# Kernel tuning notes

Measured on AMD Instinct MI355X. Metric: run time of the kernel, lower is better.

## Reference

```python
import jax, jax.numpy as jnp
import numpy as np

N = 50000      # nodes
E = 1600000    # edges (avg degree 32)
F_IN = 128
F_OUT = 64
ALPHA = 0.2    # LeakyReLU negative slope


def setup_inputs() -> dict:
    key = jax.random.key(0)
    ks = jax.random.split(key, 11)
    xav = 1.414 * (2.0 / (F_IN + F_OUT)) ** 0.5  # xavier_normal gain=1.414
    xav_a = 1.414 * (2.0 / (1 + 2 * F_OUT)) ** 0.5
    return {
        "input": jax.random.normal(ks[0], (N, F_IN), jnp.float32),
        "p_h": jax.random.normal(ks[1], (N, F_IN), jnp.float32),
        "new_h": jax.random.normal(ks[2], (N, F_IN), jnp.float32),
        "edge": jax.random.randint(ks[3], (2, E), 0, N),
        "edge_col": jax.random.randint(ks[4], (2, N), 0, N),
        "row_i": jax.random.randint(ks[5], (N,), 0, N),
        "row_resort": jax.random.randint(ks[6], (E,), 0, N),
        "adj": jnp.zeros((1,), jnp.float32),  # unused by forward (kept for signature parity)
        "W": jax.random.normal(ks[7], (F_IN, F_OUT), jnp.float32) * xav,
        "a1": jax.random.normal(ks[8], (1, 2 * F_OUT), jnp.float32) * xav_a,
        "a2": jax.random.normal(ks[9], (1, 2 * F_OUT), jnp.float32) * xav_a,
    }


def segment_softmax(src, index, num_segments):
    # torch_geometric.utils.softmax: numerically-stable softmax grouped by index
    m = jax.ops.segment_max(src, index, num_segments=num_segments)
    m = jnp.where(jnp.isfinite(m), m, 0.0)  # empty segments -> 0
    ex = jnp.exp(src - m[index])
    s = jax.ops.segment_sum(ex, index, num_segments=num_segments)
    return ex / (s[index] + 1e-16)


def reference(input, p_h, new_h, edge, edge_col, row_i, row_resort, adj, W, a1, a2):
    n = input.shape[0]
    fo = W.shape[1]
    h = input @ W            # [N, Fo]
    ph = p_h @ W             # [N, Fo]
    nh = new_h @ W           # [N, Fo]

    # a1 @ cat(h_src, p_h).T  ==  h_src @ a1_left + p_h @ a1_right  (avoids [E,2Fo] concat)
    a1l, a1r = a1[0, :fo], a1[0, fo:]
    col_score = h[edge_col[0]] @ a1l + ph @ a1r                 # [N]
    edge_col_e = jnp.exp(-jax.nn.leaky_relu(col_score, ALPHA))
    edge_col_e = segment_softmax(edge_col_e, row_i, n)

    a2l, a2r = a2[0, :fo], a2[0, fo:]
    row_score = nh[row_resort] @ a2l + h[edge[1]] @ a2r          # [E]
    edge_row_e = jnp.exp(-jax.nn.leaky_relu(row_score, ALPHA))

    edge_e = edge_row_e * edge_col_e[row_resort]                 # [E]

    # special_spmm(edge, edge_e, [N,N], ones) == segment row-sum
    e_rowsum = jax.ops.segment_sum(edge_e, edge[0], num_segments=n)[:, None]  # [N,1]
    e_rowsum = e_rowsum + jnp.where(e_rowsum == 0, 1.0, 0.0)

    attention_e = edge_e[:, None] / e_rowsum[edge[0]]            # [E,1]

    # dropout p=0.0 (eval): identity
    # special_spmm(edge, edge_e, [N,N], h) == segment-weighted aggregate
    h_prime = jax.ops.segment_sum(edge_e[:, None] * h[edge[1]], edge[0], num_segments=n)
    h_prime = h_prime / e_rowsum

    return jax.nn.elu(h_prime), edge, attention_e
```

## Files before the change

kernel.cpp:

```cpp
#include <hip/hip_runtime.h>

#define NN 50000
#define NE 1600000
#define FIN 128
#define FOUT 64
#define ALPHA 0.2f

#define RANGE 256
#define NB 196
#define EPB 2048
#define NBLK 782

__global__ void k_sniff(const int* __restrict__ edge32, int* __restrict__ iflag) {
    __shared__ int zodd;
    if (threadIdx.x == 0) zodd = 0;
    __syncthreads();
    int z = 0;
    for (int i = threadIdx.x; i < 2048; i += 256)
        if (edge32[2 * i + 1] == 0) z++;
    atomicAdd(&zodd, z);
    __syncthreads();
    if (threadIdx.x == 0) *iflag = (zodd > 2000) ? 1 : 0;
}

__device__ inline int ldi(const void* p, size_t i, int isi64) {
    int v = isi64 ? (int)((const long long*)p)[i] : ((const int*)p)[i];
    return v < 0 ? 0 : (v >= NN ? NN - 1 : v);
}

__device__ inline unsigned short f2bf(float x) {
    unsigned u = __float_as_uint(x);
    return (unsigned short)((u + 0x7FFFu + ((u >> 16) & 1u)) >> 16);
}

__global__ void k_u(const float* __restrict__ W, const float* __restrict__ a1,
                    const float* __restrict__ a2, float* __restrict__ u) {
    int k = threadIdx.x;
    float u1 = 0.f, u2 = 0.f, u3 = 0.f, u4 = 0.f;
    for (int j = 0; j < FOUT; j++) {
        float w = W[k * FOUT + j];
        u1 += w * a1[j];
        u2 += w * a1[FOUT + j];
        u3 += w * a2[j];
        u4 += w * a2[FOUT + j];
    }
    u[k] = u1; u[128 + k] = u2; u[256 + k] = u3; u[384 + k] = u4;
}

__global__ __launch_bounds__(256) void k_gemm(const float* __restrict__ X,
                                              const float* __restrict__ W,
                                              unsigned short* __restrict__ h) {
    __shared__ float wlds[FIN * FOUT];
    __shared__ float xlds[4][4][FIN];
    int tid = threadIdx.x;
    for (int i = tid; i < FIN * FOUT; i += 256) wlds[i] = W[i];
    int wave = tid >> 6, lane = tid & 63;
    int base = blockIdx.x * 16 + wave * 4;
    for (int n0 = 0; n0 < 4; n0++) {
        float2 b = ((const float2*)(X + (size_t)(base + n0) * FIN))[lane];
        xlds[wave][n0][2 * lane] = b.x;
        xlds[wave][n0][2 * lane + 1] = b.y;
    }
    __syncthreads();
    float a0 = 0.f, a1v = 0.f, a2v = 0.f, a3 = 0.f;
    for (int k = 0; k < FIN; k++) {
        float w = wlds[k * FOUT + lane];
        a0  += xlds[wave][0][k] * w;
        a1v += xlds[wave][1][k] * w;
        a2v += xlds[wave][2][k] * w;
        a3  += xlds[wave][3][k] * w;
    }
    h[(size_t)(base + 0) * FOUT + lane] = f2bf(a0);
    h[(size_t)(base + 1) * FOUT + lane] = f2bf(a1v);
    h[(size_t)(base + 2) * FOUT + lane] = f2bf(a2v);
    h[(size_t)(base + 3) * FOUT + lane] = f2bf(a3);
}

__global__ __launch_bounds__(256) void k_svec(const float* __restrict__ input,
                                              const float* __restrict__ p_h,
                                              const float* __restrict__ new_h,
                                              const float* __restrict__ u,
                                              float* __restrict__ s1, float* __restrict__ s2,
                                              float* __restrict__ sc ,
                                              float* __restrict__ s4) {
    int lane = threadIdx.x & 63;
    int v = blockIdx.x * 4 + (threadIdx.x >> 6);
    size_t row = (size_t)v * FIN;
    float2 bi = ((const float2*)(input + row))[lane];
    float2 bp = ((const float2*)(p_h   + row))[lane];
    float2 bn = ((const float2*)(new_h + row))[lane];
    float p1 = bi.x * u[2 * lane]       + bi.y * u[2 * lane + 1];
    float p2 = bp.x * u[128 + 2 * lane] + bp.y * u[128 + 2 * lane + 1];
    float p3 = bn.x * u[256 + 2 * lane] + bn.y * u[256 + 2 * lane + 1];
    float p4 = bi.x * u[384 + 2 * lane] + bi.y * u[384 + 2 * lane + 1];
#pragma unroll
    for (int off = 32; off > 0; off >>= 1) {
        p1 += __shfl_down(p1, off, 64);
        p2 += __shfl_down(p2, off, 64);
        p3 += __shfl_down(p3, off, 64);
        p4 += __shfl_down(p4, off, 64);
    }
    if (lane == 0) { s1[v] = p1; s2[v] = p2; sc[2 * v] = p3; s4[v] = p4; }
}

__global__ void k_colscore(const float* __restrict__ s1, const float* __restrict__ s2,
                           const void* __restrict__ edge_col, const void* __restrict__ row_i,
                           const int* __restrict__ iflag,
                           float* __restrict__ ec, unsigned int* __restrict__ m) {
    int i = blockIdx.x * 256 + threadIdx.x;
    if (i >= NN) return;
    int i64 = *iflag;
    float cs = s1[ldi(edge_col, i, i64)] + s2[i];
    float l = cs > 0.f ? cs : ALPHA * cs;
    float e = expf(-l);
    ec[i] = e;
    atomicMax(&m[ldi(row_i, i, i64)], __float_as_uint(e));
}

__global__ void k_expsum(float* __restrict__ ec, const unsigned int* __restrict__ m,
                         const void* __restrict__ row_i, const int* __restrict__ iflag,
                         float* __restrict__ ssum) {
    int i = blockIdx.x * 256 + threadIdx.x;
    if (i >= NN) return;
    int r = ldi(row_i, i, *iflag);
    float e = expf(ec[i] - __uint_as_float(m[r]));
    ec[i] = e;
    atomicAdd(&ssum[r], e);
}

__global__ void k_norm(const float* __restrict__ ex, const float* __restrict__ ssum,
                       const void* __restrict__ row_i, const int* __restrict__ iflag,
                       float* __restrict__ sc ) {
    int i = blockIdx.x * 256 + threadIdx.x;
    if (i >= NN) return;
    sc[2 * i + 1] = ex[i] / (ssum[ldi(row_i, i, *iflag)] + 1e-16f);
}

__global__ __launch_bounds__(512) void k_cnt(const void* __restrict__ edge,
                                             const int* __restrict__ iflag,
                                             int* __restrict__ cntm) {
    __shared__ int hist[NB];
    int tid = threadIdx.x;
    for (int t = tid; t < NB; t += 512) hist[t] = 0;
    __syncthreads();
    int i64 = *iflag;
    int base = blockIdx.x * EPB;
#pragma unroll
    for (int k = 0; k < 4; k++) {
        int e = base + k * 512 + tid;
        if (e < NE) atomicAdd(&hist[ldi(edge, e, i64) >> 8], 1);
    }
    __syncthreads();
    for (int t = tid; t < NB; t += 512)
        cntm[blockIdx.x * NB + t] = hist[t];
}

__global__ __launch_bounds__(1024) void k_colscan(const int* __restrict__ cntm,
                                                  int* __restrict__ colpre,
                                                  int* __restrict__ bcnt) {
    __shared__ int s[1024];
    int b = blockIdx.x, tid = threadIdx.x;
    int x = (tid < NBLK) ? cntm[(size_t)tid * NB + b] : 0;
    s[tid] = x;
    __syncthreads();
    for (int off = 1; off < 1024; off <<= 1) {
        int t = (tid >= off) ? s[tid - off] : 0;
        __syncthreads();
        s[tid] += t;
        __syncthreads();
    }
    if (tid < NBLK) colpre[(size_t)tid * NB + b] = s[tid] - x;
    if (tid == 1023) bcnt[b] = s[1023];
}

__global__ __launch_bounds__(256) void k_bscan(const int* __restrict__ bcnt,
                                               int* __restrict__ bstart,
                                               int* __restrict__ start) {
    __shared__ int s[256];
    int tid = threadIdx.x;
    int x = (tid < NB) ? bcnt[tid] : 0;
    s[tid] = x;
    __syncthreads();
    for (int off = 1; off < 256; off <<= 1) {
        int t = (tid >= off) ? s[tid - off] : 0;
        __syncthreads();
        s[tid] += t;
        __syncthreads();
    }
    if (tid < NB) bstart[tid] = s[tid] - x;
    if (tid == 0) { bstart[NB] = NE; start[NN] = NE; }
}

__global__ __launch_bounds__(512) void k_edgeA(const float2* __restrict__ sc, const float* __restrict__ s4,
                                               const void* __restrict__ edge, const void* __restrict__ row_resort,
                                               const int* __restrict__ iflag,
                                               const int* __restrict__ bstart, const int* __restrict__ colpre,
                                               uint2* __restrict__ tmp,
                                               float* __restrict__ edge_e ) {
    __shared__ int hist[NB];
    __shared__ int bbase[NB];
    int tid = threadIdx.x;
    for (int t = tid; t < NB; t += 512) hist[t] = 0;
    __syncthreads();
    int i64 = *iflag;
    int base = blockIdx.x * EPB;
    unsigned int key[4]; float val[4]; int rk[4], bk[4];
#pragma unroll
    for (int k = 0; k < 4; k++) {
        int e = base + k * 512 + tid;
        bk[k] = -1;
        if (e < NE) {
            int e0 = ldi(edge, e, i64);
            int e1 = ldi(edge, (size_t)NE + e, i64);
            int rr = ldi(row_resort, e, i64);
            float2 c = sc[rr];
            float rs = c.x + s4[e1];
            float l = rs > 0.f ? rs : ALPHA * rs;
            float ee = expf(-l) * c.y;
            edge_e[e] = ee;
            key[k] = (unsigned int)e0 | ((unsigned int)e1 << 16);
            val[k] = ee;
            bk[k] = e0 >> 8;
            rk[k] = atomicAdd(&hist[bk[k]], 1);
        }
    }
    __syncthreads();
    for (int t = tid; t < NB; t += 512)
        bbase[t] = bstart[t] + colpre[(size_t)blockIdx.x * NB + t];
    __syncthreads();
#pragma unroll
    for (int k = 0; k < 4; k++)
        if (bk[k] >= 0)
            tmp[bbase[bk[k]] + rk[k]] = make_uint2(key[k], __float_as_uint(val[k]));
}

__global__ __launch_bounds__(512) void k_edgeB(const uint2* __restrict__ tmp,
                                               const int* __restrict__ bstart,
                                               int* __restrict__ start,
                                               float2* __restrict__ pairs) {
    __shared__ int cnt[RANGE];
    __shared__ int s[RANGE];
    __shared__ int cur[RANGE];
    int b = blockIdx.x;
    int tid = threadIdx.x;
    int v0 = b * RANGE;
    if (tid < RANGE) cnt[tid] = 0;
    __syncthreads();
    int lo = bstart[b], hi = bstart[b + 1];
    for (int i = lo + tid; i < hi; i += 512)
        atomicAdd(&cnt[tmp[i].x & 0xFFu], 1);
    __syncthreads();
    if (tid < RANGE) s[tid] = cnt[tid];
    __syncthreads();
    for (int off = 1; off < RANGE; off <<= 1) {
        int t = 0;
        if (tid < RANGE && tid >= off) t = s[tid - off];
        __syncthreads();
        if (tid < RANGE) s[tid] += t;
        __syncthreads();
    }
    if (tid < RANGE) {
        int g = lo + s[tid] - cnt[tid];
        cur[tid] = g;
        int v = v0 + tid;
        if (v < NN) start[v] = g;
    }
    __syncthreads();
    for (int i = lo + tid; i < hi; i += 512) {
        uint2 r = tmp[i];
        int pos = atomicAdd(&cur[r.x & 0xFFu], 1);
        pairs[pos] = make_float2(__int_as_float((int)(r.x >> 16)), __uint_as_float(r.y));
    }
}

__global__ __launch_bounds__(512) void k_agg(const unsigned short* __restrict__ h,
                                             const float2* __restrict__ pairs,
                                             const int* __restrict__ start,
                                             float* __restrict__ ersum,
                                             float* __restrict__ out0) {
    int lane = threadIdx.x & 63;
    int q  = lane >> 4;
    int fq = lane & 15;
    int v = blockIdx.x * 8 + (threadIdx.x >> 6);
    int a = start[v], b = start[v + 1];
    float acc0 = 0.f, acc1 = 0.f, acc2 = 0.f, acc3 = 0.f, rs = 0.f;
    for (int j = a; j < b; j += 8) {
        int eA = j + q, eB = j + 4 + q;
        float2 pA = (eA < b) ? pairs[eA] : make_float2(__int_as_float(0), 0.f);
        float2 pB = (eB < b) ? pairs[eB] : make_float2(__int_as_float(0), 0.f);
        uint2 hA = *(const uint2*)(h + (((size_t)__float_as_int(pA.x)) << 6) + 4 * fq);
        uint2 hB = *(const uint2*)(h + (((size_t)__float_as_int(pB.x)) << 6) + 4 * fq);
        acc0 += pA.y * __uint_as_float(hA.x << 16);
        acc1 += pA.y * __uint_as_float(hA.x & 0xFFFF0000u);
        acc2 += pA.y * __uint_as_float(hA.y << 16);
        acc3 += pA.y * __uint_as_float(hA.y & 0xFFFF0000u);
        acc0 += pB.y * __uint_as_float(hB.x << 16);
        acc1 += pB.y * __uint_as_float(hB.x & 0xFFFF0000u);
        acc2 += pB.y * __uint_as_float(hB.y << 16);
        acc3 += pB.y * __uint_as_float(hB.y & 0xFFFF0000u);
        rs += pA.y + pB.y;
    }
#pragma unroll
    for (int off = 16; off <= 32; off <<= 1) {
        acc0 += __shfl_xor(acc0, off, 64);
        acc1 += __shfl_xor(acc1, off, 64);
        acc2 += __shfl_xor(acc2, off, 64);
        acc3 += __shfl_xor(acc3, off, 64);
        rs   += __shfl_xor(rs, off, 64);
    }
    if (q == 0) {
        rs += (rs == 0.f) ? 1.f : 0.f;
        float4 o;
        o.x = acc0 / rs; o.y = acc1 / rs; o.z = acc2 / rs; o.w = acc3 / rs;
        o.x = o.x > 0.f ? o.x : expm1f(o.x);
        o.y = o.y > 0.f ? o.y : expm1f(o.y);
        o.z = o.z > 0.f ? o.z : expm1f(o.z);
        o.w = o.w > 0.f ? o.w : expm1f(o.w);
        ((float4*)(out0 + (size_t)v * FOUT))[fq] = o;
        if (fq == 0) ersum[v] = rs;
    }
}

__global__ __launch_bounds__(256) void k_final(const void* __restrict__ edge, const int* __restrict__ iflag,
                                               const float* __restrict__ ersum,
                                               float* __restrict__ out2, float* __restrict__ out1) {
    int i = blockIdx.x * 256 + threadIdx.x;
    int i64 = *iflag;
    int v = i64 ? (int)((const long long*)edge)[i] : ((const int*)edge)[i];
    out1[i] = (float)v;
    if (i < NE) {
        int e0 = v < 0 ? 0 : (v >= NN ? NN - 1 : v);
        out2[i] = out2[i] / ersum[e0];
    }
}

extern "C" void kernel_launch(void* const* d_in, const int* in_sizes, int n_in,
                              void* d_out, int out_size, void* d_ws, size_t ws_size,
                              hipStream_t stream) {
    int ix[3] = {0, 1, 2}; int nx = 0;
    int iE = 3, iCol = 4, iRowI = 5, iRes = 6, iW = 8, iA1 = 9, iA2 = 10;
    bool a1seen = false;
    for (int i = 0; i < n_in; i++) {
        int s = in_sizes[i];
        if (s == NN * FIN) { if (nx < 3) ix[nx++] = i; }
        else if (s == 2 * NE) iE = i;
        else if (s == 2 * NN) iCol = i;
        else if (s == NN) iRowI = i;
        else if (s == NE) iRes = i;
        else if (s == FIN * FOUT) iW = i;
        else if (s == 2 * FOUT) { if (!a1seen) { iA1 = i; a1seen = true; } else iA2 = i; }
    }
    const float* input = (const float*)d_in[ix[0]];
    const float* p_h   = (const float*)d_in[ix[1]];
    const float* new_h = (const float*)d_in[ix[2]];
    const void* edge       = d_in[iE];
    const void* edge_col   = d_in[iCol];
    const void* row_i      = d_in[iRowI];
    const void* row_resort = d_in[iRes];
    const float* W  = (const float*)d_in[iW];
    const float* a1 = (const float*)d_in[iA1];
    const float* a2 = (const float*)d_in[iA2];

    float* out0 = (float*)d_out;
    float* out1 = out0 + (size_t)NN * FOUT;
    float* out2 = out1 + (size_t)2 * NE;

    uint2* tmp = (uint2*)out1;

    unsigned short* h = (unsigned short*)d_ws;
    float2* pairs  = (float2*)((float*)d_ws + (size_t)NN * FOUT);
    float*  s1     = (float*)(pairs + NE);
    float*  s2     = s1 + NN;
    float*  s4     = s2 + NN;
    float*  ec     = s4 + NN;
    float*  scf    = ec + NN;
    float*  mseg   = scf + 2 * (size_t)NN;
    float*  ssum   = mseg + NN;
    int*    bcnt   = (int*)(ssum + NN);
    int*    start  = bcnt + NB;
    int*    bstart = start + NN + 1;
    int*    cntm   = bstart + NB + 1;
    int*    colpre = cntm + (size_t)NBLK * NB;
    float*  ersum  = (float*)(colpre + (size_t)NBLK * NB);
    float*  u      = ersum + NN;
    int*    iflag  = (int*)(u + 512);

    hipMemsetAsync(mseg, 0, (size_t)2 * NN * sizeof(float), stream);

    k_sniff<<<1, 256, 0, stream>>>((const int*)edge, iflag);
    k_u<<<1, 128, 0, stream>>>(W, a1, a2, u);
    k_gemm<<<NN / 16, 256, 0, stream>>>(input, W, h);
    k_svec<<<NN / 4, 256, 0, stream>>>(input, p_h, new_h, u, s1, s2, scf, s4);
    k_colscore<<<(NN + 255) / 256, 256, 0, stream>>>(s1, s2, edge_col, row_i, iflag, ec, (unsigned int*)mseg);
    k_expsum<<<(NN + 255) / 256, 256, 0, stream>>>(ec, (const unsigned int*)mseg, row_i, iflag, ssum);
    k_norm<<<(NN + 255) / 256, 256, 0, stream>>>(ec, ssum, row_i, iflag, scf);
    k_cnt<<<NBLK, 512, 0, stream>>>(edge, iflag, cntm);
    k_colscan<<<NB, 1024, 0, stream>>>(cntm, colpre, bcnt);
    k_bscan<<<1, 256, 0, stream>>>(bcnt, bstart, start);
    k_edgeA<<<NBLK, 512, 0, stream>>>((const float2*)scf, s4, edge, row_resort, iflag, bstart, colpre, tmp, out2);
    k_edgeB<<<NB, 512, 0, stream>>>(tmp, bstart, start, pairs);
    k_agg<<<NN / 8, 512, 0, stream>>>(h, pairs, start, ersum, out0);
    k_final<<<2 * NE / 256, 256, 0, stream>>>(edge, iflag, ersum, out2, out1);
}
```

Before: 310.7 us.

## Merge small setup kernels, fuse edge histogram into svec, widen agg gathers

```diff
diff --git a/kernel.cpp b/kernel.cpp
--- a/kernel.cpp
+++ b/kernel.cpp
@@ -11,18 +11,6 @@
 #define EPB 2048
 #define NBLK 782
 
-__global__ void k_sniff(const int* __restrict__ edge32, int* __restrict__ iflag) {
-    __shared__ int zodd;
-    if (threadIdx.x == 0) zodd = 0;
-    __syncthreads();
-    int z = 0;
-    for (int i = threadIdx.x; i < 2048; i += 256)
-        if (edge32[2 * i + 1] == 0) z++;
-    atomicAdd(&zodd, z);
-    __syncthreads();
-    if (threadIdx.x == 0) *iflag = (zodd > 2000) ? 1 : 0;
-}
-
 __device__ inline int ldi(const void* p, size_t i, int isi64) {
     int v = isi64 ? (int)((const long long*)p)[i] : ((const int*)p)[i];
     return v < 0 ? 0 : (v >= NN ? NN - 1 : v);
@@ -33,18 +21,33 @@
     return (unsigned short)((u + 0x7FFFu + ((u >> 16) & 1u)) >> 16);
 }
 
-__global__ void k_u(const float* __restrict__ W, const float* __restrict__ a1,
-                    const float* __restrict__ a2, float* __restrict__ u) {
-    int k = threadIdx.x;
-    float u1 = 0.f, u2 = 0.f, u3 = 0.f, u4 = 0.f;
-    for (int j = 0; j < FOUT; j++) {
-        float w = W[k * FOUT + j];
-        u1 += w * a1[j];
-        u2 += w * a1[FOUT + j];
-        u3 += w * a2[j];
-        u4 += w * a2[FOUT + j];
-    }
-    u[k] = u1; u[128 + k] = u2; u[256 + k] = u3; u[384 + k] = u4;
+__global__ __launch_bounds__(256) void k_su(const int* __restrict__ edge32, int* __restrict__ iflag,
+                                            const float* __restrict__ W, const float* __restrict__ a1,
+                                            const float* __restrict__ a2, float* __restrict__ u) {
+    if (blockIdx.x == 0) {
+        __shared__ int zodd;
+        if (threadIdx.x == 0) zodd = 0;
+        __syncthreads();
+        int z = 0;
+        for (int i = threadIdx.x; i < 2048; i += 256)
+            if (edge32[2 * i + 1] == 0) z++;
+        atomicAdd(&zodd, z);
+        __syncthreads();
+        if (threadIdx.x == 0) *iflag = (zodd > 2000) ? 1 : 0;
+    } else {
+        int k = threadIdx.x;
+        if (k < FIN) {
+            float u1 = 0.f, u2 = 0.f, u3 = 0.f, u4 = 0.f;
+            for (int j = 0; j < FOUT; j++) {
+                float w = W[k * FOUT + j];
+                u1 += w * a1[j];
+                u2 += w * a1[FOUT + j];
+                u3 += w * a2[j];
+                u4 += w * a2[FOUT + j];
+            }
+            u[k] = u1; u[128 + k] = u2; u[256 + k] = u3; u[384 + k] = u4;
+        }
+    }
 }
 
 __global__ __launch_bounds__(256) void k_gemm(const float* __restrict__ X,
@@ -76,31 +79,52 @@
     h[(size_t)(base + 3) * FOUT + lane] = f2bf(a3);
 }
 
-__global__ __launch_bounds__(256) void k_svec(const float* __restrict__ input,
-                                              const float* __restrict__ p_h,
-                                              const float* __restrict__ new_h,
-                                              const float* __restrict__ u,
-                                              float* __restrict__ s1, float* __restrict__ s2,
-                                              float* __restrict__ sc ,
-                                              float* __restrict__ s4) {
-    int lane = threadIdx.x & 63;
-    int v = blockIdx.x * 4 + (threadIdx.x >> 6);
-    size_t row = (size_t)v * FIN;
-    float2 bi = ((const float2*)(input + row))[lane];
-    float2 bp = ((const float2*)(p_h   + row))[lane];
-    float2 bn = ((const float2*)(new_h + row))[lane];
-    float p1 = bi.x * u[2 * lane]       + bi.y * u[2 * lane + 1];
-    float p2 = bp.x * u[128 + 2 * lane] + bp.y * u[128 + 2 * lane + 1];
-    float p3 = bn.x * u[256 + 2 * lane] + bn.y * u[256 + 2 * lane + 1];
-    float p4 = bi.x * u[384 + 2 * lane] + bi.y * u[384 + 2 * lane + 1];
+__global__ __launch_bounds__(256) void k_svec_cnt(const float* __restrict__ input,
+                                                  const float* __restrict__ p_h,
+                                                  const float* __restrict__ new_h,
+                                                  const float* __restrict__ u,
+                                                  float* __restrict__ s1, float* __restrict__ s2,
+                                                  float* __restrict__ sc ,
+                                                  float* __restrict__ s4,
+                                                  const void* __restrict__ edge,
+                                                  const int* __restrict__ iflag,
+                                                  int* __restrict__ cntm) {
+    __shared__ int hist[NB];
+    int tid = threadIdx.x;
+    if (blockIdx.x < 12500) {
+        int lane = tid & 63;
+        int v = blockIdx.x * 4 + (tid >> 6);
+        size_t row = (size_t)v * FIN;
+        float2 bi = ((const float2*)(input + row))[lane];
+        float2 bp = ((const float2*)(p_h   + row))[lane];
+        float2 bn = ((const float2*)(new_h + row))[lane];
+        float p1 = bi.x * u[2 * lane]       + bi.y * u[2 * lane + 1];
+        float p2 = bp.x * u[128 + 2 * lane] + bp.y * u[128 + 2 * lane + 1];
+        float p3 = bn.x * u[256 + 2 * lane] + bn.y * u[256 + 2 * lane + 1];
+        float p4 = bi.x * u[384 + 2 * lane] + bi.y * u[384 + 2 * lane + 1];
 #pragma unroll
-    for (int off = 32; off > 0; off >>= 1) {
-        p1 += __shfl_down(p1, off, 64);
-        p2 += __shfl_down(p2, off, 64);
-        p3 += __shfl_down(p3, off, 64);
-        p4 += __shfl_down(p4, off, 64);
-    }
-    if (lane == 0) { s1[v] = p1; s2[v] = p2; sc[2 * v] = p3; s4[v] = p4; }
+        for (int off = 32; off > 0; off >>= 1) {
+            p1 += __shfl_down(p1, off, 64);
+            p2 += __shfl_down(p2, off, 64);
+            p3 += __shfl_down(p3, off, 64);
+            p4 += __shfl_down(p4, off, 64);
+        }
+        if (lane == 0) { s1[v] = p1; s2[v] = p2; sc[2 * v] = p3; s4[v] = p4; }
+    } else {
+        int cb = blockIdx.x - 12500;
+        for (int t = tid; t < NB; t += 256) hist[t] = 0;
+        __syncthreads();
+        int i64 = *iflag;
+        int base = cb * EPB;
+#pragma unroll
+        for (int k = 0; k < 8; k++) {
+            int e = base + k * 256 + tid;
+            if (e < NE) atomicAdd(&hist[ldi(edge, e, i64) >> 8], 1);
+        }
+        __syncthreads();
+        for (int t = tid; t < NB; t += 256)
+            cntm[cb * NB + t] = hist[t];
+    }
 }
 
 __global__ void k_colscore(const float* __restrict__ s1, const float* __restrict__ s2,
@@ -134,25 +158,6 @@
     int i = blockIdx.x * 256 + threadIdx.x;
     if (i >= NN) return;
     sc[2 * i + 1] = ex[i] / (ssum[ldi(row_i, i, *iflag)] + 1e-16f);
-}
-
-__global__ __launch_bounds__(512) void k_cnt(const void* __restrict__ edge,
-                                             const int* __restrict__ iflag,
-                                             int* __restrict__ cntm) {
-    __shared__ int hist[NB];
-    int tid = threadIdx.x;
-    for (int t = tid; t < NB; t += 512) hist[t] = 0;
-    __syncthreads();
-    int i64 = *iflag;
-    int base = blockIdx.x * EPB;
-#pragma unroll
-    for (int k = 0; k < 4; k++) {
-        int e = base + k * 512 + tid;
-        if (e < NE) atomicAdd(&hist[ldi(edge, e, i64) >> 8], 1);
-    }
-    __syncthreads();
-    for (int t = tid; t < NB; t += 512)
-        cntm[blockIdx.x * NB + t] = hist[t];
 }
 
 __global__ __launch_bounds__(1024) void k_colscan(const int* __restrict__ cntm,
@@ -279,44 +284,89 @@
                                              float* __restrict__ ersum,
                                              float* __restrict__ out0) {
     int lane = threadIdx.x & 63;
-    int q  = lane >> 4;
-    int fq = lane & 15;
+    int q  = lane >> 3;
+    int fq = lane & 7;
     int v = blockIdx.x * 8 + (threadIdx.x >> 6);
     int a = start[v], b = start[v + 1];
-    float acc0 = 0.f, acc1 = 0.f, acc2 = 0.f, acc3 = 0.f, rs = 0.f;
-    for (int j = a; j < b; j += 8) {
-        int eA = j + q, eB = j + 4 + q;
-        float2 pA = (eA < b) ? pairs[eA] : make_float2(__int_as_float(0), 0.f);
-        float2 pB = (eB < b) ? pairs[eB] : make_float2(__int_as_float(0), 0.f);
-        uint2 hA = *(const uint2*)(h + (((size_t)__float_as_int(pA.x)) << 6) + 4 * fq);
-        uint2 hB = *(const uint2*)(h + (((size_t)__float_as_int(pB.x)) << 6) + 4 * fq);
+    float acc0 = 0.f, acc1 = 0.f, acc2 = 0.f, acc3 = 0.f;
+    float acc4 = 0.f, acc5 = 0.f, acc6 = 0.f, acc7 = 0.f, rs = 0.f;
+    int bfull = a + ((b - a) & ~15);
+    int j = a;
+    for (; j < bfull; j += 16) {
+        float2 pA = pairs[j + q];
+        float2 pB = pairs[j + 8 + q];
+        uint4 hA = *(const uint4*)(h + (((size_t)__float_as_int(pA.x)) << 6) + 8 * fq);
+        uint4 hB = *(const uint4*)(h + (((size_t)__float_as_int(pB.x)) << 6) + 8 * fq);
         acc0 += pA.y * __uint_as_float(hA.x << 16);
         acc1 += pA.y * __uint_as_float(hA.x & 0xFFFF0000u);
         acc2 += pA.y * __uint_as_float(hA.y << 16);
         acc3 += pA.y * __uint_as_float(hA.y & 0xFFFF0000u);
+        acc4 += pA.y * __uint_as_float(hA.z << 16);
+        acc5 += pA.y * __uint_as_float(hA.z & 0xFFFF0000u);
+        acc6 += pA.y * __uint_as_float(hA.w << 16);
+        acc7 += pA.y * __uint_as_float(hA.w & 0xFFFF0000u);
         acc0 += pB.y * __uint_as_float(hB.x << 16);
         acc1 += pB.y * __uint_as_float(hB.x & 0xFFFF0000u);
         acc2 += pB.y * __uint_as_float(hB.y << 16);
         acc3 += pB.y * __uint_as_float(hB.y & 0xFFFF0000u);
+        acc4 += pB.y * __uint_as_float(hB.z << 16);
+        acc5 += pB.y * __uint_as_float(hB.z & 0xFFFF0000u);
+        acc6 += pB.y * __uint_as_float(hB.w << 16);
+        acc7 += pB.y * __uint_as_float(hB.w & 0xFFFF0000u);
         rs += pA.y + pB.y;
     }
+    if (j < b) {
+        int eA = j + q, eB = j + 8 + q;
+        float2 pA = (eA < b) ? pairs[eA] : make_float2(__int_as_float(0), 0.f);
+        float2 pB = (eB < b) ? pairs[eB] : make_float2(__int_as_float(0), 0.f);
+        uint4 hA = *(const uint4*)(h + (((size_t)__float_as_int(pA.x)) << 6) + 8 * fq);
+        uint4 hB = *(const uint4*)(h + (((size_t)__float_as_int(pB.x)) << 6) + 8 * fq);
+        acc0 += pA.y * __uint_as_float(hA.x << 16);
+        acc1 += pA.y * __uint_as_float(hA.x & 0xFFFF0000u);
+        acc2 += pA.y * __uint_as_float(hA.y << 16);
+        acc3 += pA.y * __uint_as_float(hA.y & 0xFFFF0000u);
+        acc4 += pA.y * __uint_as_float(hA.z << 16);
+        acc5 += pA.y * __uint_as_float(hA.z & 0xFFFF0000u);
+        acc6 += pA.y * __uint_as_float(hA.w << 16);
+        acc7 += pA.y * __uint_as_float(hA.w & 0xFFFF0000u);
+        acc0 += pB.y * __uint_as_float(hB.x << 16);
+        acc1 += pB.y * __uint_as_float(hB.x & 0xFFFF0000u);
+        acc2 += pB.y * __uint_as_float(hB.y << 16);
+        acc3 += pB.y * __uint_as_float(hB.y & 0xFFFF0000u);
+        acc4 += pB.y * __uint_as_float(hB.z << 16);
+        acc5 += pB.y * __uint_as_float(hB.z & 0xFFFF0000u);
+        acc6 += pB.y * __uint_as_float(hB.w << 16);
+        acc7 += pB.y * __uint_as_float(hB.w & 0xFFFF0000u);
+        rs += pA.y + pB.y;
+    }
 #pragma unroll
-    for (int off = 16; off <= 32; off <<= 1) {
+    for (int off = 8; off <= 32; off <<= 1) {
         acc0 += __shfl_xor(acc0, off, 64);
         acc1 += __shfl_xor(acc1, off, 64);
         acc2 += __shfl_xor(acc2, off, 64);
         acc3 += __shfl_xor(acc3, off, 64);
+        acc4 += __shfl_xor(acc4, off, 64);
+        acc5 += __shfl_xor(acc5, off, 64);
+        acc6 += __shfl_xor(acc6, off, 64);
+        acc7 += __shfl_xor(acc7, off, 64);
         rs   += __shfl_xor(rs, off, 64);
     }
     if (q == 0) {
         rs += (rs == 0.f) ? 1.f : 0.f;
-        float4 o;
-        o.x = acc0 / rs; o.y = acc1 / rs; o.z = acc2 / rs; o.w = acc3 / rs;
-        o.x = o.x > 0.f ? o.x : expm1f(o.x);
-        o.y = o.y > 0.f ? o.y : expm1f(o.y);
-        o.z = o.z > 0.f ? o.z : expm1f(o.z);
-        o.w = o.w > 0.f ? o.w : expm1f(o.w);
-        ((float4*)(out0 + (size_t)v * FOUT))[fq] = o;
+        float4 o1, o2;
+        o1.x = acc0 / rs; o1.y = acc1 / rs; o1.z = acc2 / rs; o1.w = acc3 / rs;
+        o2.x = acc4 / rs; o2.y = acc5 / rs; o2.z = acc6 / rs; o2.w = acc7 / rs;
+        o1.x = o1.x > 0.f ? o1.x : expm1f(o1.x);
+        o1.y = o1.y > 0.f ? o1.y : expm1f(o1.y);
+        o1.z = o1.z > 0.f ? o1.z : expm1f(o1.z);
+        o1.w = o1.w > 0.f ? o1.w : expm1f(o1.w);
+        o2.x = o2.x > 0.f ? o2.x : expm1f(o2.x);
+        o2.y = o2.y > 0.f ? o2.y : expm1f(o2.y);
+        o2.z = o2.z > 0.f ? o2.z : expm1f(o2.z);
+        o2.w = o2.w > 0.f ? o2.w : expm1f(o2.w);
+        float4* dst = (float4*)(out0 + (size_t)v * FOUT + 8 * fq);
+        dst[0] = o1;
+        dst[1] = o2;
         if (fq == 0) ersum[v] = rs;
     }
 }
@@ -387,14 +437,13 @@
 
     hipMemsetAsync(mseg, 0, (size_t)2 * NN * sizeof(float), stream);
 
-    k_sniff<<<1, 256, 0, stream>>>((const int*)edge, iflag);
-    k_u<<<1, 128, 0, stream>>>(W, a1, a2, u);
+    k_su<<<2, 256, 0, stream>>>((const int*)edge, iflag, W, a1, a2, u);
     k_gemm<<<NN / 16, 256, 0, stream>>>(input, W, h);
-    k_svec<<<NN / 4, 256, 0, stream>>>(input, p_h, new_h, u, s1, s2, scf, s4);
+    k_svec_cnt<<<12500 + NBLK, 256, 0, stream>>>(input, p_h, new_h, u, s1, s2, scf, s4,
+                                                 edge, iflag, cntm);
     k_colscore<<<(NN + 255) / 256, 256, 0, stream>>>(s1, s2, edge_col, row_i, iflag, ec, (unsigned int*)mseg);
     k_expsum<<<(NN + 255) / 256, 256, 0, stream>>>(ec, (const unsigned int*)mseg, row_i, iflag, ssum);
     k_norm<<<(NN + 255) / 256, 256, 0, stream>>>(ec, ssum, row_i, iflag, scf);
-    k_cnt<<<NBLK, 512, 0, stream>>>(edge, iflag, cntm);
     k_colscan<<<NB, 1024, 0, stream>>>(cntm, colpre, bcnt);
     k_bscan<<<1, 256, 0, stream>>>(bcnt, bstart, start);
     k_edgeA<<<NBLK, 512, 0, stream>>>((const float2*)scf, s4, edge, row_resort, iflag, bstart, colpre, tmp, out2);
```

Result: faster. 297.4 us (-4.3%).
